# Kernel optimization log

Hardware: AMD Instinct MI355X
Metric: run time of the kernel (lower is better)

## Reference

```python
import jax, jax.numpy as jnp
import numpy as np

INPUT_DIM1 = 512
INPUT_DIM2 = 512
OUTPUT_DIM = 8192


def _make_sketch(seed_h, seed_s, input_dim, output_dim):
    # Faithful to torch module: dense [input_dim, output_dim] matrix with one
    # nonzero (+-1) per row at column rand_h[i].
    np.random.seed(seed_h)
    rand_h = np.random.randint(output_dim, size=input_dim)
    np.random.seed(seed_s)
    rand_s = (2 * np.random.randint(2, size=input_dim) - 1).astype(np.float32)
    M = np.zeros((input_dim, output_dim), dtype=np.float32)
    M[np.arange(input_dim), rand_h] = rand_s
    return jnp.asarray(M)


def setup_inputs() -> dict:
    key = jax.random.key(0)
    k1, k2 = jax.random.split(key)
    bottom1 = jax.random.normal(k1, (32, INPUT_DIM1, 14, 14), dtype=jnp.float32)
    bottom2 = jax.random.normal(k2, (32, INPUT_DIM2, 14, 14), dtype=jnp.float32)
    S1 = _make_sketch(1, 3, INPUT_DIM1, OUTPUT_DIM)
    S2 = _make_sketch(5, 7, INPUT_DIM2, OUTPUT_DIM)
    return {"bottom1": bottom1, "bottom2": bottom2, "S1": S1, "S2": S2}


def reference(bottom1, bottom2, S1, S2):
    B, _, H, W = bottom1.shape
    d = S1.shape[1]
    # [B, C, H, W] -> [B*H*W, C]
    b1 = jnp.transpose(bottom1, (0, 2, 3, 1)).reshape(-1, bottom1.shape[1])
    b2 = jnp.transpose(bottom2, (0, 2, 3, 1)).reshape(-1, bottom2.shape[1])
    sketch1 = b1 @ S1  # [N, d]
    sketch2 = b2 @ S2
    fft1 = jnp.fft.fft(sketch1, axis=-1)
    fft2 = jnp.fft.fft(sketch2, axis=-1)
    cbp_flat = jnp.real(jnp.fft.ifft(fft1 * fft2, axis=-1))
    cbp = cbp_flat.reshape(B, H, W, d)
    return cbp.sum(axis=(1, 2))  # sum_pool=True -> [B, d]
```

## Files before the change

### kernel.cpp

```cpp
#include <hip/hip_runtime.h>


#define D     8192
#define DMASK 8191
#define C     512
#define HW    196
#define NB    32
#define NCH   7
#define NSL   16

typedef __attribute__((ext_vector_type(8))) short bf16x8;
typedef __attribute__((ext_vector_type(4))) float f32x4;

__device__ __forceinline__ unsigned short f2bf(float f) {
    unsigned u = __float_as_uint(f);
    return (unsigned short)((u + 0x7fffu + ((u >> 16) & 1u)) >> 16);
}

__device__ __forceinline__ bf16x8 pack8(float4 a, float4 b) {
    bf16x8 r;
    r[0] = (short)f2bf(a.x); r[1] = (short)f2bf(a.y);
    r[2] = (short)f2bf(a.z); r[3] = (short)f2bf(a.w);
    r[4] = (short)f2bf(b.x); r[5] = (short)f2bf(b.y);
    r[6] = (short)f2bf(b.z); r[7] = (short)f2bf(b.w);
    return r;
}

__global__ __launch_bounds__(256) void extract2(
    const float* __restrict__ S1, const float* __restrict__ S2,
    int* __restrict__ h1, float* __restrict__ s1,
    int* __restrict__ h2, float* __restrict__ s2)
{
    const int  row   = blockIdx.x & 511;
    const bool first = blockIdx.x < 512;
    const float* S = first ? S1 : S2;
    const float4* rp = (const float4*)(S + (size_t)row * D);
    const int tid = threadIdx.x;

    float4 v[8];
    #pragma unroll
    for (int ii = 0; ii < 8; ++ii) v[ii] = rp[tid + 256 * ii];

    float ssum = 0.f, wsum = 0.f;
    #pragma unroll
    for (int ii = 0; ii < 8; ++ii) {
        const float base = (float)(4 * (tid + 256 * ii));
        ssum += (v[ii].x + v[ii].y) + (v[ii].z + v[ii].w);
        wsum += v[ii].x * base + v[ii].y * (base + 1.f)
              + v[ii].z * (base + 2.f) + v[ii].w * (base + 3.f);
    }
    #pragma unroll
    for (int off = 32; off; off >>= 1) {
        ssum += __shfl_down(ssum, off, 64);
        wsum += __shfl_down(wsum, off, 64);
    }
    __shared__ float rs[4], rw[4];
    if ((tid & 63) == 0) { rs[tid >> 6] = ssum; rw[tid >> 6] = wsum; }
    __syncthreads();
    if (tid == 0) {
        const float st = (rs[0] + rs[1]) + (rs[2] + rs[3]);
        const float wt = (rw[0] + rw[1]) + (rw[2] + rw[3]);
        if (first) { h1[row] = (int)(wt * st); s1[row] = st; }
        else       { h2[row] = (int)(wt * st); s2[row] = st; }
    }
}

__global__ __launch_bounds__(256, 2) void cbp_mfma(
    const float* __restrict__ b1, const float* __restrict__ b2,
    const int* __restrict__ h1, const float* __restrict__ s1,
    const int* __restrict__ h2, const float* __restrict__ s2,
    float* __restrict__ P)
{
    const int b  = blockIdx.z;
    const int t1 = blockIdx.y;
    const int t2 = blockIdx.x;

    __shared__ float hist[D];
    __shared__ int   h1t[128], h2t[128];
    __shared__ float s1t[128], s2t[128];

    const int tid = threadIdx.x;

    #pragma unroll
    for (int i = 0; i < 8; ++i) {
        float4 z = {0.f, 0.f, 0.f, 0.f};
        ((float4*)hist)[tid + 256 * i] = z;
    }
    if (tid < 128) {
        h1t[tid] = h1[t1 * 128 + tid];  s1t[tid] = s1[t1 * 128 + tid];
        h2t[tid] = h2[t2 * 128 + tid];  s2t[tid] = s2[t2 * 128 + tid];
    }

    const int lane  = tid & 63;
    const int w     = tid >> 6;
    const int ln15  = lane & 15;
    const int qd    = lane >> 4;
    const int koff  = qd * 8;
    const int mbase = (w >> 1) * 64;
    const int nbase = (w & 1) * 64;

    const float* Ap[4];
    const float* Bp[4];
    #pragma unroll
    for (int i = 0; i < 4; ++i) {
        Ap[i] = b1 + ((size_t)b * C + t1 * 128 + mbase + i * 16 + ln15) * HW + koff;
        Bp[i] = b2 + ((size_t)b * C + t2 * 128 + nbase + i * 16 + ln15) * HW + koff;
    }

    f32x4 acc[4][4] = {};

    float4 la[8], lb[8];
    #pragma unroll
    for (int i = 0; i < 4; ++i) {
        la[2 * i]     = *(const float4*)(Ap[i]);
        la[2 * i + 1] = *(const float4*)(Ap[i] + 4);
        lb[2 * i]     = *(const float4*)(Bp[i]);
        lb[2 * i + 1] = *(const float4*)(Bp[i] + 4);
    }

    #pragma unroll
    for (int ch = 0; ch < NCH; ++ch) {
        float4 na[8], nb[8];
        if (ch + 1 < NCH) {
            const int base = (ch + 1) * 32;
            const bool v0 = (base + koff + 4) <= HW;
            const bool v1 = (base + koff + 8) <= HW;
            const float4 z = {0.f, 0.f, 0.f, 0.f};
            #pragma unroll
            for (int i = 0; i < 4; ++i) {
                na[2 * i]     = v0 ? *(const float4*)(Ap[i] + base)     : z;
                na[2 * i + 1] = v1 ? *(const float4*)(Ap[i] + base + 4) : z;
                nb[2 * i]     = v0 ? *(const float4*)(Bp[i] + base)     : z;
                nb[2 * i + 1] = v1 ? *(const float4*)(Bp[i] + base + 4) : z;
            }
        }

        bf16x8 av[4], bv[4];
        #pragma unroll
        for (int i = 0; i < 4; ++i) {
            av[i] = pack8(la[2 * i], la[2 * i + 1]);
            bv[i] = pack8(lb[2 * i], lb[2 * i + 1]);
        }
        #pragma unroll
        for (int i = 0; i < 4; ++i)
            #pragma unroll
            for (int j = 0; j < 4; ++j)
                acc[i][j] = __builtin_amdgcn_mfma_f32_16x16x32_bf16(
                    av[i], bv[j], acc[i][j], 0, 0, 0);

        if (ch + 1 < NCH) {
            #pragma unroll
            for (int t = 0; t < 8; ++t) { la[t] = na[t]; lb[t] = nb[t]; }
        }
    }

    __syncthreads();

    int   p2v[4]; float q2[4];
    #pragma unroll
    for (int j = 0; j < 4; ++j) {
        const int cc = nbase + j * 16 + ln15;
        p2v[j] = h2t[cc];  q2[j] = s2t[cc];
    }
    #pragma unroll
    for (int i = 0; i < 4; ++i) {
        #pragma unroll
        for (int qq = 0; qq < 4; ++qq) {
            const int rw2 = mbase + i * 16 + qd * 4 + qq;
            const int   p1 = h1t[rw2];
            const float sr = s1t[rw2];
            #pragma unroll
            for (int j = 0; j < 4; ++j)
                atomicAdd(&hist[(p1 + p2v[j]) & DMASK],
                          acc[i][j][qq] * sr * q2[j]);
        }
    }

    __syncthreads();

    float* Pslice = P + (size_t)(b * NSL + t1 * 4 + t2) * D;
    #pragma unroll
    for (int i = 0; i < 8; ++i)
        ((float4*)Pslice)[tid + 256 * i] = ((const float4*)hist)[tid + 256 * i];
}

__global__ __launch_bounds__(256) void reduce16(
    const float* __restrict__ P, float* __restrict__ out)
{
    const int idx4 = blockIdx.x * 256 + threadIdx.x;
    const int b    = idx4 >> 11;
    const int d4   = idx4 & 2047;

    const float4* base = (const float4*)(P + (size_t)b * NSL * D) + d4;
    float4 v[NSL];
    #pragma unroll
    for (int s = 0; s < NSL; ++s) v[s] = base[s * (D / 4)];

    float4 acc = v[0];
    #pragma unroll
    for (int s = 1; s < NSL; ++s) {
        acc.x += v[s].x; acc.y += v[s].y; acc.z += v[s].z; acc.w += v[s].w;
    }
    ((float4*)out)[idx4] = acc;
}

extern "C" void kernel_launch(void* const* d_in, const int* in_sizes, int n_in,
                              void* d_out, int out_size, void* d_ws, size_t ws_size,
                              hipStream_t stream)
{
    const float* bottom1 = (const float*)d_in[0];
    const float* bottom2 = (const float*)d_in[1];
    const float* S1      = (const float*)d_in[2];
    const float* S2      = (const float*)d_in[3];
    float* out = (float*)d_out;

    float* P  = (float*)d_ws;
    int*   h1 = (int*)(P + (size_t)NB * NSL * D);
    int*   h2 = h1 + C;
    float* s1 = (float*)(h2 + C);
    float* s2 = s1 + C;

    extract2<<<1024, 256, 0, stream>>>(S1, S2, h1, s1, h2, s2);
    cbp_mfma<<<dim3(4, 4, NB), 256, 0, stream>>>(bottom1, bottom2,
                                                 h1, s1, h2, s2, P);
    reduce16<<<256, 256, 0, stream>>>(P, out);
}
```

Baseline: 163.2 us.

## Stage bf16 tiles through LDS with halved M tile and sign folded into conversion

Result: no change. 164.1 us (+0.6%).

```diff
diff --git a/kernel.cpp b/kernel.cpp
--- a/kernel.cpp
+++ b/kernel.cpp
@@ -6,24 +6,16 @@
 #define C     512
 #define HW    196
 #define NB    32
+#define LDK   40
 #define NCH   7
-#define NSL   16
+#define NSL   32
 
 typedef __attribute__((ext_vector_type(8))) short bf16x8;
 typedef __attribute__((ext_vector_type(4))) float f32x4;
 
-__device__ __forceinline__ unsigned short f2bf(float f) {
-    unsigned u = __float_as_uint(f);
+__device__ __forceinline__ unsigned short f2bf(float f, unsigned xm) {
+    unsigned u = __float_as_uint(f) ^ xm;
     return (unsigned short)((u + 0x7fffu + ((u >> 16) & 1u)) >> 16);
-}
-
-__device__ __forceinline__ bf16x8 pack8(float4 a, float4 b) {
-    bf16x8 r;
-    r[0] = (short)f2bf(a.x); r[1] = (short)f2bf(a.y);
-    r[2] = (short)f2bf(a.z); r[3] = (short)f2bf(a.w);
-    r[4] = (short)f2bf(b.x); r[5] = (short)f2bf(b.y);
-    r[6] = (short)f2bf(b.z); r[7] = (short)f2bf(b.w);
-    return r;
 }
 
 __global__ __launch_bounds__(256) void extract2(
@@ -65,19 +57,22 @@
     }
 }
 
-__global__ __launch_bounds__(256, 2) void cbp_mfma(
+__global__ __launch_bounds__(256, 3) void cbp_mfma(
     const float* __restrict__ b1, const float* __restrict__ b2,
     const int* __restrict__ h1, const float* __restrict__ s1,
     const int* __restrict__ h2, const float* __restrict__ s2,
     float* __restrict__ P)
 {
-    const int b  = blockIdx.z;
-    const int t1 = blockIdx.y;
-    const int t2 = blockIdx.x;
+    const int id = blockIdx.x;
+    const int b  = id & 31;
+    const int m  = id >> 5;
+    const int t1 = m >> 2;
+    const int t2 = m & 3;
 
     __shared__ float hist[D];
-    __shared__ int   h1t[128], h2t[128];
-    __shared__ float s1t[128], s2t[128];
+    __shared__ __align__(16) unsigned short As[64 * LDK];
+    __shared__ __align__(16) unsigned short Bs[128 * LDK];
+    __shared__ int h1t[64], h2t[128];
 
     const int tid = threadIdx.x;
 
@@ -86,105 +81,113 @@
         float4 z = {0.f, 0.f, 0.f, 0.f};
         ((float4*)hist)[tid + 256 * i] = z;
     }
-    if (tid < 128) {
-        h1t[tid] = h1[t1 * 128 + tid];  s1t[tid] = s1[t1 * 128 + tid];
-        h2t[tid] = h2[t2 * 128 + tid];  s2t[tid] = s2[t2 * 128 + tid];
-    }
+    if (tid < 64)  h1t[tid] = h1[t1 * 64 + tid];
+    if (tid < 128) h2t[tid] = h2[t2 * 128 + tid];
+
+    const int ra = tid >> 2;
+    const int ka = (tid & 3) * 8;
+    const int rb = tid >> 1;
+    const int kb = (tid & 1) * 16;
+
+    const float* Abase = b1 + ((size_t)b * C + t1 * 64 + ra) * HW;
+    const float* Bbase = b2 + ((size_t)b * C + t2 * 128 + rb) * HW;
+
+    const unsigned am = (s1[t1 * 64  + ra] < 0.f) ? 0x80000000u : 0u;
+    const unsigned bm = (s2[t2 * 128 + rb] < 0.f) ? 0x80000000u : 0u;
+
+    float4 pva[2], pvb[4];
+    pva[0] = *(const float4*)(Abase + ka);
+    pva[1] = *(const float4*)(Abase + ka + 4);
+    #pragma unroll
+    for (int t = 0; t < 4; ++t)
+        pvb[t] = *(const float4*)(Bbase + kb + 4 * t);
 
     const int lane  = tid & 63;
     const int w     = tid >> 6;
     const int ln15  = lane & 15;
     const int qd    = lane >> 4;
     const int koff  = qd * 8;
-    const int mbase = (w >> 1) * 64;
+    const int mbase = (w >> 1) * 32;
     const int nbase = (w & 1) * 64;
 
-    const float* Ap[4];
-    const float* Bp[4];
-    #pragma unroll
-    for (int i = 0; i < 4; ++i) {
-        Ap[i] = b1 + ((size_t)b * C + t1 * 128 + mbase + i * 16 + ln15) * HW + koff;
-        Bp[i] = b2 + ((size_t)b * C + t2 * 128 + nbase + i * 16 + ln15) * HW + koff;
-    }
-
-    f32x4 acc[4][4] = {};
-
-    float4 la[8], lb[8];
-    #pragma unroll
-    for (int i = 0; i < 4; ++i) {
-        la[2 * i]     = *(const float4*)(Ap[i]);
-        la[2 * i + 1] = *(const float4*)(Ap[i] + 4);
-        lb[2 * i]     = *(const float4*)(Bp[i]);
-        lb[2 * i + 1] = *(const float4*)(Bp[i] + 4);
-    }
-
-    #pragma unroll
+    f32x4 acc[2][4] = {};
+
     for (int ch = 0; ch < NCH; ++ch) {
-        float4 na[8], nb[8];
-        if (ch + 1 < NCH) {
-            const int base = (ch + 1) * 32;
-            const bool v0 = (base + koff + 4) <= HW;
-            const bool v1 = (base + koff + 8) <= HW;
-            const float4 z = {0.f, 0.f, 0.f, 0.f};
-            #pragma unroll
-            for (int i = 0; i < 4; ++i) {
-                na[2 * i]     = v0 ? *(const float4*)(Ap[i] + base)     : z;
-                na[2 * i + 1] = v1 ? *(const float4*)(Ap[i] + base + 4) : z;
-                nb[2 * i]     = v0 ? *(const float4*)(Bp[i] + base)     : z;
-                nb[2 * i + 1] = v1 ? *(const float4*)(Bp[i] + base + 4) : z;
+        {
+            uint2 u0, u1;
+            u0.x = (unsigned)f2bf(pva[0].x, am) | ((unsigned)f2bf(pva[0].y, am) << 16);
+            u0.y = (unsigned)f2bf(pva[0].z, am) | ((unsigned)f2bf(pva[0].w, am) << 16);
+            u1.x = (unsigned)f2bf(pva[1].x, am) | ((unsigned)f2bf(pva[1].y, am) << 16);
+            u1.y = (unsigned)f2bf(pva[1].z, am) | ((unsigned)f2bf(pva[1].w, am) << 16);
+            *(uint2*)&As[ra * LDK + ka]     = u0;
+            *(uint2*)&As[ra * LDK + ka + 4] = u1;
+            #pragma unroll
+            for (int t = 0; t < 2; ++t) {
+                uint2 ub;
+                ub.x = (unsigned)f2bf(pvb[2*t].x, bm) | ((unsigned)f2bf(pvb[2*t].y, bm) << 16);
+                ub.y = (unsigned)f2bf(pvb[2*t].z, bm) | ((unsigned)f2bf(pvb[2*t].w, bm) << 16);
+                *(uint2*)&Bs[rb * LDK + kb + 8 * t] = ub;
+                uint2 uc;
+                uc.x = (unsigned)f2bf(pvb[2*t+1].x, bm) | ((unsigned)f2bf(pvb[2*t+1].y, bm) << 16);
+                uc.y = (unsigned)f2bf(pvb[2*t+1].z, bm) | ((unsigned)f2bf(pvb[2*t+1].w, bm) << 16);
+                *(uint2*)&Bs[rb * LDK + kb + 8 * t + 4] = uc;
             }
         }
-
-        bf16x8 av[4], bv[4];
-        #pragma unroll
-        for (int i = 0; i < 4; ++i) {
-            av[i] = pack8(la[2 * i], la[2 * i + 1]);
-            bv[i] = pack8(lb[2 * i], lb[2 * i + 1]);
+        __syncthreads();
+
+        if (ch + 1 < NCH) {
+            const int gk = (ch + 1) * 32;
+            const float4 z = {0.f, 0.f, 0.f, 0.f};
+            const int gka = gk + ka;
+            pva[0] = (gka + 4 <= HW) ? *(const float4*)(Abase + gka)     : z;
+            pva[1] = (gka + 8 <= HW) ? *(const float4*)(Abase + gka + 4) : z;
+            #pragma unroll
+            for (int t = 0; t < 4; ++t) {
+                const int gkb = gk + kb + 4 * t;
+                pvb[t] = (gkb + 4 <= HW) ? *(const float4*)(Bbase + gkb) : z;
+            }
         }
-        #pragma unroll
-        for (int i = 0; i < 4; ++i)
+
+        bf16x8 av[2], bv[4];
+        #pragma unroll
+        for (int i = 0; i < 2; ++i)
+            av[i] = *(const bf16x8*)&As[(mbase + i * 16 + ln15) * LDK + koff];
+        #pragma unroll
+        for (int j = 0; j < 4; ++j)
+            bv[j] = *(const bf16x8*)&Bs[(nbase + j * 16 + ln15) * LDK + koff];
+        #pragma unroll
+        for (int i = 0; i < 2; ++i)
             #pragma unroll
             for (int j = 0; j < 4; ++j)
                 acc[i][j] = __builtin_amdgcn_mfma_f32_16x16x32_bf16(
                     av[i], bv[j], acc[i][j], 0, 0, 0);
-
-        if (ch + 1 < NCH) {
-            #pragma unroll
-            for (int t = 0; t < 8; ++t) { la[t] = na[t]; lb[t] = nb[t]; }
+        __syncthreads();
+    }
+
+    int p2v[4];
+    #pragma unroll
+    for (int j = 0; j < 4; ++j)
+        p2v[j] = h2t[nbase + j * 16 + ln15];
+
+    #pragma unroll
+    for (int i = 0; i < 2; ++i)
+        #pragma unroll
+        for (int qq = 0; qq < 4; ++qq) {
+            const int p1 = h1t[mbase + i * 16 + qd * 4 + qq];
+            #pragma unroll
+            for (int j = 0; j < 4; ++j)
+                atomicAdd(&hist[(p1 + p2v[j]) & DMASK], acc[i][j][qq]);
         }
-    }
 
     __syncthreads();
 
-    int   p2v[4]; float q2[4];
-    #pragma unroll
-    for (int j = 0; j < 4; ++j) {
-        const int cc = nbase + j * 16 + ln15;
-        p2v[j] = h2t[cc];  q2[j] = s2t[cc];
-    }
-    #pragma unroll
-    for (int i = 0; i < 4; ++i) {
-        #pragma unroll
-        for (int qq = 0; qq < 4; ++qq) {
-            const int rw2 = mbase + i * 16 + qd * 4 + qq;
-            const int   p1 = h1t[rw2];
-            const float sr = s1t[rw2];
-            #pragma unroll
-            for (int j = 0; j < 4; ++j)
-                atomicAdd(&hist[(p1 + p2v[j]) & DMASK],
-                          acc[i][j][qq] * sr * q2[j]);
-        }
-    }
-
-    __syncthreads();
-
-    float* Pslice = P + (size_t)(b * NSL + t1 * 4 + t2) * D;
+    float* Pslice = P + (size_t)(b * NSL + m) * D;
     #pragma unroll
     for (int i = 0; i < 8; ++i)
         ((float4*)Pslice)[tid + 256 * i] = ((const float4*)hist)[tid + 256 * i];
 }
 
-__global__ __launch_bounds__(256) void reduce16(
+__global__ __launch_bounds__(256) void reduce32(
     const float* __restrict__ P, float* __restrict__ out)
 {
     const int idx4 = blockIdx.x * 256 + threadIdx.x;
@@ -192,14 +195,11 @@
     const int d4   = idx4 & 2047;
 
     const float4* base = (const float4*)(P + (size_t)b * NSL * D) + d4;
-    float4 v[NSL];
-    #pragma unroll
-    for (int s = 0; s < NSL; ++s) v[s] = base[s * (D / 4)];
-
-    float4 acc = v[0];
+    float4 acc = base[0];
     #pragma unroll
     for (int s = 1; s < NSL; ++s) {
-        acc.x += v[s].x; acc.y += v[s].y; acc.z += v[s].z; acc.w += v[s].w;
+        float4 v = base[s * (D / 4)];
+        acc.x += v.x; acc.y += v.y; acc.z += v.z; acc.w += v.w;
     }
     ((float4*)out)[idx4] = acc;
 }
@@ -221,7 +221,7 @@
     float* s2 = s1 + C;
 
     extract2<<<1024, 256, 0, stream>>>(S1, S2, h1, s1, h2, s2);
-    cbp_mfma<<<dim3(4, 4, NB), 256, 0, stream>>>(bottom1, bottom2,
-                                                 h1, s1, h2, s2, P);
-    reduce16<<<256, 256, 0, stream>>>(P, out);
-}
+    cbp_mfma<<<1024, 256, 0, stream>>>(bottom1, bottom2,
+                                       h1, s1, h2, s2, P);
+    reduce32<<<256, 256, 0, stream>>>(P, out);
+}
```
